# Kernel optimization log

Hardware: AMD Instinct MI355X
Metric: run time of the kernel (lower is better)

The kernel has to match this reference:

```python
import jax, jax.numpy as jnp
import numpy as np
from jax import lax

M, G = 16, 4
INP = 256
OUP = 256
K = 3
EPS = 1e-5


def _weightnet(x, gap_vec, fc1_w, fc1_b, fc2_w, inp, oup, stride):
    # x: [B, inp, H, W], gap_vec: [B, 16]
    B, _, H, W = x.shape
    a = jax.nn.sigmoid(gap_vec @ fc1_w.T + fc1_b)          # [B, M*oup]
    groups = G * oup                                        # 1024
    out_pg = (oup * inp * K * K) // groups                  # 576
    in_pg = (M * oup) // groups                             # 4
    a = a.reshape(B, groups, in_pg)
    w2 = fc2_w.reshape(groups, out_pg, in_pg)
    # grouped 1x1 conv generating per-sample conv weights
    xw = jnp.einsum('bgi,goi->bgo', a, w2)                  # [B, groups, out_pg]
    xw = xw.reshape(B * oup, inp, K, K)                     # per-sample kernels
    xr = x.reshape(1, B * inp, H, W)
    out = lax.conv_general_dilated(
        xr, xw, (stride, stride), [(1, 1), (1, 1)],
        dimension_numbers=('NCHW', 'OIHW', 'NCHW'),
        feature_group_count=B)
    return out.reshape(B, oup, out.shape[2], out.shape[3])


def _bn(x, g, b, m, v):
    scale = (g / jnp.sqrt(v + EPS))[:, None, None]
    return (x - m[:, None, None]) * scale + b[:, None, None]


def setup_inputs() -> dict:
    key = jax.random.key(0)
    ks = jax.random.split(key, 20)
    d = {}
    d['x'] = jax.random.normal(ks[0], (32, 256, 56, 56), jnp.float32)
    d['reduce_w'] = jax.random.normal(ks[1], (16, 256), jnp.float32) * 0.05
    d['reduce_b'] = jax.random.normal(ks[2], (16,), jnp.float32) * 0.05
    d['w1_fc1_w'] = jax.random.normal(ks[3], (4096, 16), jnp.float32) * 0.05
    d['w1_fc1_b'] = jax.random.normal(ks[4], (4096,), jnp.float32) * 0.05
    d['w1_fc2_w'] = jax.random.normal(ks[5], (589824, 4), jnp.float32) * 0.05
    d['bn1_g'] = jax.random.uniform(ks[6], (256,), jnp.float32) + 0.5
    d['bn1_b'] = jax.random.normal(ks[7], (256,), jnp.float32) * 0.05
    d['bn1_m'] = jax.random.normal(ks[8], (256,), jnp.float32) * 0.05
    d['bn1_v'] = jax.random.uniform(ks[9], (256,), jnp.float32) + 0.5
    d['w2_fc1_w'] = jax.random.normal(ks[10], (4096, 16), jnp.float32) * 0.05
    d['w2_fc1_b'] = jax.random.normal(ks[11], (4096,), jnp.float32) * 0.05
    d['w2_fc2_w'] = jax.random.normal(ks[12], (589824, 4), jnp.float32) * 0.05
    d['bn2_g'] = jax.random.uniform(ks[13], (256,), jnp.float32) + 0.5
    d['bn2_b'] = jax.random.normal(ks[14], (256,), jnp.float32) * 0.05
    d['bn2_m'] = jax.random.normal(ks[15], (256,), jnp.float32) * 0.05
    d['bn2_v'] = jax.random.uniform(ks[16], (256,), jnp.float32) + 0.5
    return d


def reference(x, reduce_w, reduce_b, w1_fc1_w, w1_fc1_b, w1_fc2_w,
              bn1_g, bn1_b, bn1_m, bn1_v,
              w2_fc1_w, w2_fc1_b, w2_fc2_w,
              bn2_g, bn2_b, bn2_m, bn2_v):
    # global average pool -> reduce 1x1 conv
    gap = x.mean(axis=(2, 3))                       # [B, in_planes]
    gap = gap @ reduce_w.T + reduce_b               # [B, 16]
    out = _weightnet(x, gap, w1_fc1_w, w1_fc1_b, w1_fc2_w, INP, OUP, 1)
    out = jax.nn.relu(_bn(out, bn1_g, bn1_b, bn1_m, bn1_v))
    out = _weightnet(out, gap, w2_fc1_w, w2_fc1_b, w2_fc2_w, OUP, OUP, 1)
    out = _bn(out, bn2_g, bn2_b, bn2_m, bn2_v)
    out = out + x                                   # identity shortcut (stride=1, in==out)
    return jax.nn.relu(out)
```

## Files before the change

kernel.cpp:

```cpp
#include <hip/hip_runtime.h>

typedef short bf16x8 __attribute__((ext_vector_type(8)));
typedef float f32x4 __attribute__((ext_vector_type(4)));

#define EPSV 1e-5f
#define BNUM 32
#define CH 256
#define HW 3136
#define PXT 3684
#define NCHUNK 32
#define PERB_SHORTS (NCHUNK*PXT*8)
#define WB_PERB 589824

__device__ __forceinline__ unsigned short f2bf(float f) {
  unsigned int u = __float_as_uint(f);
  u += 0x7fffu + ((u >> 16) & 1u);
  return (unsigned short)(u >> 16);
}

__device__ __forceinline__ void gld16(const void* g, void* l) {
  __builtin_amdgcn_global_load_lds((const __attribute__((address_space(1))) void*)g,
                                   (__attribute__((address_space(3))) void*)l,
                                   16, 0, 0);
}

__global__ void k_gap16(const float* __restrict__ gapc, const float* __restrict__ rw,
                        const float* __restrict__ rb, float* __restrict__ g16) {
  int b = blockIdx.x;
  int t = threadIdx.x;
  int j = t >> 5;
  int c0 = t & 31;
  const float* gc = gapc + b * 256;
  const float* w = rw + j * 256;
  float s = 0.f;
#pragma unroll
  for (int k = 0; k < 8; ++k) s += gc[c0 + k * 32] * w[c0 + k * 32];
  for (int off = 16; off; off >>= 1) s += __shfl_down(s, off, 32);
  if (c0 == 0) g16[b * 16 + j] = s * (1.f / 3136.f) + rb[j];
}

__global__ void k_act(const float* __restrict__ g16,
                      const float* __restrict__ w1w, const float* __restrict__ w1b,
                      const float* __restrict__ w2w, const float* __restrict__ w2b,
                      float* __restrict__ a1, float* __restrict__ a2) {
  int idx = blockIdx.x * 256 + threadIdx.x;
  int which = idx >> 17;
  int r = idx & 131071;
  int b = r >> 12, m = r & 4095;
  const float* w = (which ? w2w : w1w) + m * 16;
  float s = which ? w2b[m] : w1b[m];
  const float* g = g16 + b * 16;
#pragma unroll
  for (int j = 0; j < 16; ++j) s += g[j] * w[j];
  float out = 1.f / (1.f + __expf(-s));
  (which ? a2 : a1)[r] = out;
}

__global__ void k_zero(unsigned short* __restrict__ xp1, unsigned short* __restrict__ xp2) {
  int bc = blockIdx.x;
  int t = threadIdx.x;
  uint4 z = {0u, 0u, 0u, 0u};
  for (int wbuf = 0; wbuf < 2; ++wbuf) {
    unsigned short* base = (wbuf ? xp2 : xp1) + (size_t)bc * (PXT * 8);
    uint4* p = (uint4*)base;
    if (t < 123) p[t] = z;
    p[3370 + t] = z;
    if (t < 58) p[3626 + t] = z;
    if (t < 56) {
      int e = 64 + (t + 1) * 58 + 57;
      p[e] = z;
      p[e + 1] = z;
    }
  }
}

__global__ void k_xpad(const float* __restrict__ x, unsigned short* __restrict__ xp,
                       float* __restrict__ gapc) {
  int y = blockIdx.x, ch = blockIdx.y, b = blockIdx.z;
  int l = threadIdx.x;
  bool act = (l < 56);
  int lc = act ? l : 0;
  const float* src = x + ((size_t)(b * 256 + ch * 8)) * HW + y * 56 + lc;
  float v[8];
#pragma unroll
  for (int k = 0; k < 8; ++k) v[k] = act ? src[k * HW] : 0.f;
  if (act) {
    ushort4 lo, hi;
    lo.x = f2bf(v[0]); lo.y = f2bf(v[1]); lo.z = f2bf(v[2]); lo.w = f2bf(v[3]);
    hi.x = f2bf(v[4]); hi.y = f2bf(v[5]); hi.z = f2bf(v[6]); hi.w = f2bf(v[7]);
    unsigned short* dst = xp + ((size_t)(b * NCHUNK + ch)) * (PXT * 8)
                             + (size_t)(64 + (y + 1) * 58 + (l + 1)) * 8;
    *(ushort4*)dst = lo;
    *(ushort4*)(dst + 4) = hi;
  }
#pragma unroll
  for (int k = 0; k < 8; ++k) {
    float s = v[k];
    for (int off = 32; off; off >>= 1) s += __shfl_down(s, off, 64);
    if (l == 0) atomicAdd(&gapc[b * 256 + ch * 8 + k], s);
  }
}

__global__ void k_wgen(const float* __restrict__ a, const float4* __restrict__ w2,
                       unsigned short* __restrict__ wb) {
  int og = blockIdx.x & 63, bg = blockIdx.x >> 6;
  int t = threadIdx.x;
  for (int it = 0; it < 36; ++it) {
    int wi = it * 256 + t;
    int oc_l = wi / 2304;
    int r = wi - oc_l * 2304;
    int ic = r / 9;
    int k9 = r - ic * 9;
    int kh = k9 / 3;
    int kw = k9 - kh * 3;
    int oc = og * 4 + oc_l;
    int g = oc * 4 + (ic >> 6);
    int o = (ic & 63) * 9 + k9;
    float4 w4 = w2[g * 576 + o];
    int s_ = ic >> 5, kc_ = (ic >> 3) & 3, icl = ic & 7;
    int ocg_ = oc >> 7, ocl_ = oc & 127;
    size_t off = (size_t)((kh * 8 + s_) * 2 + ocg_) * 12288 + kc_ * 3072 + ocl_ * 24
               + kw * 8 + icl;
#pragma unroll
    for (int bi = 0; bi < 4; ++bi) {
      int b = bg * 4 + bi;
      float4 a4 = *(const float4*)(a + b * 4096 + g * 4);
      float s = w4.x * a4.x + w4.y * a4.y + w4.z * a4.z + w4.w * a4.w;
      wb[(size_t)b * WB_PERB + off] = f2bf(s);
    }
  }
}

__global__ __launch_bounds__(256, 2)
void k_conv(const unsigned short* __restrict__ xpad,
            const unsigned short* __restrict__ wbuf,
            const float* __restrict__ bgp, const float* __restrict__ bbp,
            const float* __restrict__ bmp, const float* __restrict__ bvp,
            const float* __restrict__ resid,
            unsigned short* __restrict__ outpad,
            float* __restrict__ outf,
            const int mode) {
  __shared__ unsigned short sW[2][12288];
  __shared__ unsigned short sX[12288];

  const int tid = threadIdx.x;
  const int lane = tid & 63;
  const int wv = tid >> 6;
  const int wocg = wv >> 1;
  const int wpxg = wv & 1;
  const int ocl = lane & 15;
  const int kc = lane >> 4;

  int rid = blockIdx.x;
  int xcd = rid & 7;
  int j = rid >> 3;
  int b = xcd + 8 * (j / 30);
  int slot = j % 30;
  int bocg = slot & 1;
  int p0 = 58 + (slot >> 1) * 224;

  const unsigned short* xb = xpad + (size_t)b * PERB_SHORTS + 64 * 8;
  const unsigned short* wbb = wbuf + (size_t)b * WB_PERB + bocg * 12288;

  f32x4 acc[4][7];
#pragma unroll
  for (int i = 0; i < 4; ++i)
#pragma unroll
    for (int k = 0; k < 7; ++k)
      acc[i][k] = (f32x4){0.f, 0.f, 0.f, 0.f};

  auto STAGE_W = [&](int t, int buf) {
    int s = t / 3;
    int kh = t - s * 3;
    const unsigned short* wsrc = wbb + (size_t)(kh * 8 + s) * 24576;
#pragma unroll
    for (int i = 0; i < 6; ++i) {
      int seg = wv * 6 + i;
      gld16(wsrc + seg * 512 + lane * 8, &sW[buf][seg * 512]);
    }
  };
  auto STAGE_X = [&](int s) {
    const unsigned short* xs = xb + ((long)(s * 4 + wv) * PXT + p0 - 59) * 8;
#pragma unroll
    for (int i = 0; i < 6; ++i)
      gld16(xs + (i * 64 + lane) * 8, &sX[wv * 3072 + i * 512]);
  };

  STAGE_X(0);
  STAGE_W(0, 0);
  int cur = 0;
  for (int s8 = 0; s8 < 8; ++s8) {
    asm volatile("s_waitcnt vmcnt(0)" ::: "memory");
    __builtin_amdgcn_s_barrier();
#pragma unroll
    for (int kh = 0; kh < 3; ++kh) {
      int t = s8 * 3 + kh;
      if (t + 1 < 24) {
        STAGE_W(t + 1, cur ^ 1);
        asm volatile("s_waitcnt vmcnt(6)" ::: "memory");
      } else {
        asm volatile("s_waitcnt vmcnt(0)" ::: "memory");
      }
      __builtin_amdgcn_s_barrier();
#pragma unroll
      for (int kw = 0; kw < 3; ++kw) {
        bf16x8 af[4], bfr[7];
#pragma unroll
        for (int fm = 0; fm < 4; ++fm)
          af[fm] = *(const bf16x8*)&sW[cur][kc * 3072 + (wocg * 64 + fm * 16 + ocl) * 24 + kw * 8];
#pragma unroll
        for (int fn = 0; fn < 7; ++fn)
          bfr[fn] = *(const bf16x8*)&sX[kc * 3072 + (kh * 58 + wpxg * 112 + fn * 16 + ocl + kw) * 8];
        __builtin_amdgcn_s_setprio(1);
#pragma unroll
        for (int fm = 0; fm < 4; ++fm)
#pragma unroll
          for (int fn = 0; fn < 7; ++fn)
            acc[fm][fn] = __builtin_amdgcn_mfma_f32_16x16x32_bf16(af[fm], bfr[fn], acc[fm][fn], 0, 0, 0);
        __builtin_amdgcn_s_setprio(0);
      }
      __builtin_amdgcn_s_barrier();
      if (kh == 2 && s8 + 1 < 8) STAGE_X(s8 + 1);
      cur ^= 1;
    }
  }

  float* scb = (float*)&sX[0];
  if (tid < 128) {
    int oc = bocg * 128 + tid;
    float sc = bgp[oc] * rsqrtf(bvp[oc] + EPSV);
    scb[tid] = sc;
    scb[128 + tid] = bbp[oc] - bmp[oc] * sc;
  }
  __syncthreads();

  const int dpb = wpxg * 112 + ocl;
  if (mode == 1) {
#pragma unroll
    for (int fn = 0; fn < 7; ++fn) {
      int pp = p0 + dpb + fn * 16;
      int py = pp / 58;
      int px = pp - py * 58;
      if (py < 1 || py > 56 || px < 1 || px > 56) continue;
#pragma unroll
      for (int fm = 0; fm < 4; ++fm) {
        int loc = wocg * 64 + fm * 16 + kc * 4;
        f32x4 v = acc[fm][fn];
        ushort4 w;
        w.x = f2bf(fmaxf(v[0] * scb[loc + 0] + scb[128 + loc + 0], 0.f));
        w.y = f2bf(fmaxf(v[1] * scb[loc + 1] + scb[128 + loc + 1], 0.f));
        w.z = f2bf(fmaxf(v[2] * scb[loc + 2] + scb[128 + loc + 2], 0.f));
        w.w = f2bf(fmaxf(v[3] * scb[loc + 3] + scb[128 + loc + 3], 0.f));
        int ocg_g = bocg * 128 + loc;
        *(ushort4*)&outpad[((size_t)(b * NCHUNK + (ocg_g >> 3))) * (PXT * 8)
                           + (size_t)(64 + pp) * 8 + (ocg_g & 7)] = w;
      }
    }
  } else {
#pragma unroll
    for (int fn = 0; fn < 7; ++fn) {
      int pp = p0 + dpb + fn * 16;
      int py = pp / 58;
      int px = pp - py * 58;
      if (py < 1 || py > 56 || px < 1 || px > 56) continue;
      int obase = (py - 1) * 56 + (px - 1);
#pragma unroll
      for (int fm = 0; fm < 4; ++fm) {
        int loc = wocg * 64 + fm * 16 + kc * 4;
        f32x4 v = acc[fm][fn];
#pragma unroll
        for (int r = 0; r < 4; ++r) {
          int oc = bocg * 128 + loc + r;
          size_t oi = ((size_t)(b * CH + oc)) * HW + obase;
          float tv = v[r] * scb[loc + r] + scb[128 + loc + r] + resid[oi];
          outf[oi] = fmaxf(tv, 0.f);
        }
      }
    }
  }
}

#define OFF_XP1 ((size_t)0)
#define XP_BYTES ((size_t)BNUM * PERB_SHORTS * 2)
#define OFF_XP2 (OFF_XP1 + XP_BYTES)
#define OFF_WB  (OFF_XP2 + XP_BYTES)
#define WB_BYTES ((size_t)BNUM * WB_PERB * 2)
#define OFF_GAPC (OFF_WB + WB_BYTES)
#define OFF_G16  (OFF_GAPC + 32768)
#define OFF_A1   (OFF_G16 + 2048)
#define OFF_A2   (OFF_A1 + 524288)

extern "C" void kernel_launch(void* const* d_in, const int* in_sizes, int n_in,
                              void* d_out, int out_size, void* d_ws, size_t ws_size,
                              hipStream_t stream) {
  (void)in_sizes; (void)n_in; (void)out_size; (void)ws_size;
  const float* x        = (const float*)d_in[0];
  const float* reduce_w = (const float*)d_in[1];
  const float* reduce_b = (const float*)d_in[2];
  const float* w1fc1w   = (const float*)d_in[3];
  const float* w1fc1b   = (const float*)d_in[4];
  const float* w1fc2w   = (const float*)d_in[5];
  const float* bn1g     = (const float*)d_in[6];
  const float* bn1b     = (const float*)d_in[7];
  const float* bn1m     = (const float*)d_in[8];
  const float* bn1v     = (const float*)d_in[9];
  const float* w2fc1w   = (const float*)d_in[10];
  const float* w2fc1b   = (const float*)d_in[11];
  const float* w2fc2w   = (const float*)d_in[12];
  const float* bn2g     = (const float*)d_in[13];
  const float* bn2b     = (const float*)d_in[14];
  const float* bn2m     = (const float*)d_in[15];
  const float* bn2v     = (const float*)d_in[16];

  char* ws = (char*)d_ws;
  unsigned short* xp1 = (unsigned short*)(ws + OFF_XP1);
  unsigned short* xp2 = (unsigned short*)(ws + OFF_XP2);
  unsigned short* wb  = (unsigned short*)(ws + OFF_WB);
  float* gapc = (float*)(ws + OFF_GAPC);
  float* g16  = (float*)(ws + OFF_G16);
  float* a1   = (float*)(ws + OFF_A1);
  float* a2   = (float*)(ws + OFF_A2);
  float* outf = (float*)d_out;

  hipMemsetAsync(gapc, 0, 32 * 256 * 4, stream);
  k_zero<<<1024, 256, 0, stream>>>(xp1, xp2);
  k_xpad<<<dim3(56, NCHUNK, BNUM), 64, 0, stream>>>(x, xp1, gapc);
  k_gap16<<<BNUM, 512, 0, stream>>>(gapc, reduce_w, reduce_b, g16);
  k_act<<<1024, 256, 0, stream>>>(g16, w1fc1w, w1fc1b, w2fc1w, w2fc1b, a1, a2);

  k_wgen<<<512, 256, 0, stream>>>(a1, (const float4*)w1fc2w, wb);
  k_conv<<<960, 256, 0, stream>>>(xp1, wb, bn1g, bn1b, bn1m, bn1v,
                                  nullptr, xp2, nullptr, 1);
  k_wgen<<<512, 256, 0, stream>>>(a2, (const float4*)w2fc2w, wb);
  k_conv<<<960, 256, 0, stream>>>(xp2, wb, bn2g, bn2b, bn2m, bn2v,
                                  x, nullptr, outf, 2);
}
```

Before: 472.0 us.

## Split GAP into its own reduction kernel and restructure conv barriers and X staging

Global average pooling moves out of the padding kernel into a dedicated per-channel reduction kernel with float4 loads. This removes the atomics and the memset, and the mean scaling is applied there instead of in the reduce step. The conv main loop now does an explicit lgkmcnt wait and a sched_barrier before the MFMAs and a barrier after each kw step. X staging is hoisted to after the kh loop, and the initial waitcnt and barrier move outside the loop. The extra GAP kernel reads x a second time, and the per-kw barriers add synchronisation that may cost more than they save.

```diff
diff --git a/kernel.cpp b/kernel.cpp
--- a/kernel.cpp
+++ b/kernel.cpp
@@ -22,6 +22,23 @@
   __builtin_amdgcn_global_load_lds((const __attribute__((address_space(1))) void*)g,
                                    (__attribute__((address_space(3))) void*)l,
                                    16, 0, 0);
+}
+
+__global__ void k_gapc(const float* __restrict__ x, float* __restrict__ gapc) {
+  int bc = blockIdx.x;
+  const float4* p4 = (const float4*)(x + (size_t)bc * HW);
+  int t = threadIdx.x;
+  float s = 0.f;
+  for (int i = t; i < 784; i += 256) {
+    float4 v = p4[i];
+    s += v.x + v.y + v.z + v.w;
+  }
+  for (int off = 32; off; off >>= 1) s += __shfl_down(s, off, 64);
+  __shared__ float red[4];
+  int lane = t & 63, wv = t >> 6;
+  if (lane == 0) red[wv] = s;
+  __syncthreads();
+  if (t == 0) gapc[bc] = (red[0] + red[1] + red[2] + red[3]) * (1.f / 3136.f);
 }
 
 __global__ void k_gap16(const float* __restrict__ gapc, const float* __restrict__ rw,
@@ -36,7 +53,7 @@
 #pragma unroll
   for (int k = 0; k < 8; ++k) s += gc[c0 + k * 32] * w[c0 + k * 32];
   for (int off = 16; off; off >>= 1) s += __shfl_down(s, off, 32);
-  if (c0 == 0) g16[b * 16 + j] = s * (1.f / 3136.f) + rb[j];
+  if (c0 == 0) g16[b * 16 + j] = s + rb[j];
 }
 
 __global__ void k_act(const float* __restrict__ g16,
@@ -74,31 +91,20 @@
   }
 }
 
-__global__ void k_xpad(const float* __restrict__ x, unsigned short* __restrict__ xp,
-                       float* __restrict__ gapc) {
+__global__ void k_xpad(const float* __restrict__ x, unsigned short* __restrict__ xp) {
   int y = blockIdx.x, ch = blockIdx.y, b = blockIdx.z;
   int l = threadIdx.x;
-  bool act = (l < 56);
-  int lc = act ? l : 0;
-  const float* src = x + ((size_t)(b * 256 + ch * 8)) * HW + y * 56 + lc;
-  float v[8];
-#pragma unroll
-  for (int k = 0; k < 8; ++k) v[k] = act ? src[k * HW] : 0.f;
-  if (act) {
-    ushort4 lo, hi;
-    lo.x = f2bf(v[0]); lo.y = f2bf(v[1]); lo.z = f2bf(v[2]); lo.w = f2bf(v[3]);
-    hi.x = f2bf(v[4]); hi.y = f2bf(v[5]); hi.z = f2bf(v[6]); hi.w = f2bf(v[7]);
-    unsigned short* dst = xp + ((size_t)(b * NCHUNK + ch)) * (PXT * 8)
-                             + (size_t)(64 + (y + 1) * 58 + (l + 1)) * 8;
-    *(ushort4*)dst = lo;
-    *(ushort4*)(dst + 4) = hi;
-  }
-#pragma unroll
-  for (int k = 0; k < 8; ++k) {
-    float s = v[k];
-    for (int off = 32; off; off >>= 1) s += __shfl_down(s, off, 64);
-    if (l == 0) atomicAdd(&gapc[b * 256 + ch * 8 + k], s);
-  }
+  if (l >= 56) return;
+  const float* src = x + ((size_t)(b * 256 + ch * 8)) * HW + y * 56 + l;
+  ushort4 lo, hi;
+  lo.x = f2bf(src[0 * HW]); lo.y = f2bf(src[1 * HW]);
+  lo.z = f2bf(src[2 * HW]); lo.w = f2bf(src[3 * HW]);
+  hi.x = f2bf(src[4 * HW]); hi.y = f2bf(src[5 * HW]);
+  hi.z = f2bf(src[6 * HW]); hi.w = f2bf(src[7 * HW]);
+  unsigned short* dst = xp + ((size_t)(b * NCHUNK + ch)) * (PXT * 8)
+                           + (size_t)(64 + (y + 1) * 58 + (l + 1)) * 8;
+  *(ushort4*)dst = lo;
+  *(ushort4*)(dst + 4) = hi;
 }
 
 __global__ void k_wgen(const float* __restrict__ a, const float4* __restrict__ w2,
@@ -188,10 +194,11 @@
 
   STAGE_X(0);
   STAGE_W(0, 0);
+  asm volatile("s_waitcnt vmcnt(0)" ::: "memory");
+  __builtin_amdgcn_s_barrier();
+
   int cur = 0;
   for (int s8 = 0; s8 < 8; ++s8) {
-    asm volatile("s_waitcnt vmcnt(0)" ::: "memory");
-    __builtin_amdgcn_s_barrier();
 #pragma unroll
     for (int kh = 0; kh < 3; ++kh) {
       int t = s8 * 3 + kh;
@@ -211,6 +218,8 @@
 #pragma unroll
         for (int fn = 0; fn < 7; ++fn)
           bfr[fn] = *(const bf16x8*)&sX[kc * 3072 + (kh * 58 + wpxg * 112 + fn * 16 + ocl + kw) * 8];
+        asm volatile("s_waitcnt lgkmcnt(0)" ::: "memory");
+        __builtin_amdgcn_sched_barrier(0);
         __builtin_amdgcn_s_setprio(1);
 #pragma unroll
         for (int fm = 0; fm < 4; ++fm)
@@ -218,11 +227,11 @@
           for (int fn = 0; fn < 7; ++fn)
             acc[fm][fn] = __builtin_amdgcn_mfma_f32_16x16x32_bf16(af[fm], bfr[fn], acc[fm][fn], 0, 0, 0);
         __builtin_amdgcn_s_setprio(0);
+        __builtin_amdgcn_s_barrier();
       }
-      __builtin_amdgcn_s_barrier();
-      if (kh == 2 && s8 + 1 < 8) STAGE_X(s8 + 1);
       cur ^= 1;
     }
+    if (s8 + 1 < 8) STAGE_X(s8 + 1);
   }
 
   float* scb = (float*)&sX[0];
@@ -322,11 +331,11 @@
   float* a2   = (float*)(ws + OFF_A2);
   float* outf = (float*)d_out;
 
-  hipMemsetAsync(gapc, 0, 32 * 256 * 4, stream);
-  k_zero<<<1024, 256, 0, stream>>>(xp1, xp2);
-  k_xpad<<<dim3(56, NCHUNK, BNUM), 64, 0, stream>>>(x, xp1, gapc);
+  k_gapc<<<BNUM * CH, 256, 0, stream>>>(x, gapc);
   k_gap16<<<BNUM, 512, 0, stream>>>(gapc, reduce_w, reduce_b, g16);
   k_act<<<1024, 256, 0, stream>>>(g16, w1fc1w, w1fc1b, w2fc1w, w2fc1b, a1, a2);
+  k_zero<<<1024, 256, 0, stream>>>(xp1, xp2);
+  k_xpad<<<dim3(56, NCHUNK, BNUM), 64, 0, stream>>>(x, xp1);
 
   k_wgen<<<512, 256, 0, stream>>>(a1, (const float4*)w1fc2w, wb);
   k_conv<<<960, 256, 0, stream>>>(xp1, wb, bn1g, bn1b, bn1m, bn1v,
```

New measurement: 405.4 us. -14.1%, faster.
